# Optimization experiments

Measured on AMD Instinct MI355X. Metric: run time of the kernel, lower is better.

Reference implementation:

```python
import jax, jax.numpy as jnp
import numpy as np

B, N, D_IN, D_OUT = 2, 4096, 768, 768


def setup_inputs() -> dict:
    key = jax.random.key(0)
    kx, kq, kk, kv = jax.random.split(key, 4)
    x = jax.random.normal(kx, (B, N, D_IN), dtype=jnp.float32)
    # Linear(d_in, d_out, bias=False) weights, stored as [d_in, d_out]
    scale = 1.0 / np.sqrt(D_IN)
    Wq = jax.random.normal(kq, (D_IN, D_OUT), dtype=jnp.float32) * scale
    Wk = jax.random.normal(kk, (D_IN, D_OUT), dtype=jnp.float32) * scale
    Wv = jax.random.normal(kv, (D_IN, D_OUT), dtype=jnp.float32) * scale
    return {"x": x, "Wq": Wq, "Wk": Wk, "Wv": Wv}


def reference(x, Wq, Wk, Wv):
    # q,k,v: [B, N, D_OUT]
    q = jnp.einsum('bnd,de->bne', x, Wq)
    k = jnp.einsum('bnd,de->bne', x, Wk)
    v = jnp.einsum('bnd,de->bne', x, Wv)
    # Full [B, N, N] score matrix (naive attention, as in source).
    # NOTE: source's masked_fill is non-in-place and discarded, so NO causal
    # mask is actually applied -- reproduced faithfully here.
    scores = jnp.einsum('bqe,bke->bqk', q, k) / jnp.sqrt(jnp.float32(k.shape[-1]))
    weights = jax.nn.softmax(scores, axis=-1)
    # dropout rate 0.0 / eval mode -> identity
    out = jnp.einsum('bqk,bke->bqe', weights, v)  # [B, N, D_OUT]
    return out
```

## Files before the change

kernel.cpp:

```cpp
#include <hip/hip_runtime.h>

typedef __bf16 bf16x8 __attribute__((ext_vector_type(8)));
typedef float f32x4 __attribute__((ext_vector_type(4)));
typedef unsigned short us8 __attribute__((ext_vector_type(8)));

#define GAS __attribute__((address_space(1)))
#define LAS __attribute__((address_space(3)))

__device__ __forceinline__ unsigned short f32_to_bf16(float f) {
    unsigned int u = __float_as_uint(f);
    u += 0x7FFFu + ((u >> 16) & 1u);
    return (unsigned short)(u >> 16);
}

__device__ __forceinline__ float bf16_to_f32(unsigned short h) {
    return __uint_as_float((unsigned int)h << 16);
}

__device__ __forceinline__ void load16(const unsigned short* g, unsigned short* l) {
    __builtin_amdgcn_global_load_lds((GAS unsigned int*)g, (LAS unsigned int*)l, 16, 0, 0);
}

__global__ __launch_bounds__(1024) void prep(
    const float* __restrict__ x, unsigned short* __restrict__ Xbf,
    const float* __restrict__ W0, const float* __restrict__ W1, const float* __restrict__ W2,
    unsigned short* __restrict__ T0, unsigned short* __restrict__ T1, unsigned short* __restrict__ T2)
{
    __shared__ float tile[32][33];
    const int id = blockIdx.x;
    const int t = threadIdx.x;
    if (id < 1536) {
        int i = id * 1024 + t;
        float4 v = ((const float4*)x)[i];
        ushort4 o;
        o.x = f32_to_bf16(v.x); o.y = f32_to_bf16(v.y);
        o.z = f32_to_bf16(v.z); o.w = f32_to_bf16(v.w);
        ((ushort4*)Xbf)[i] = o;
    } else {
        const int tid = id - 1536;
        const int z = tid / 576, rem = tid % 576;
        const int by = rem / 24, bx = rem % 24;
        const float* W = (z == 0) ? W0 : (z == 1) ? W1 : W2;
        unsigned short* T = (z == 0) ? T0 : (z == 1) ? T1 : T2;
        const int r0 = by * 32, c0 = bx * 32;
        const int tx = t & 31, ty = t >> 5;
        tile[ty][tx] = W[(size_t)(r0 + ty) * 768 + c0 + tx];
        __syncthreads();
        T[(size_t)(c0 + ty) * 768 + r0 + tx] = f32_to_bf16(tile[tx][ty]);
    }
}

template <typename CT>
__global__ __launch_bounds__(256) void gemm_nt(
    const unsigned short* __restrict__ A, const unsigned short* __restrict__ B,
    CT* __restrict__ C, int K, int lda, int ldb, int ldc,
    size_t sA, size_t sB, size_t sC, float alpha)
{
    A += (size_t)blockIdx.z * sA;
    B += (size_t)blockIdx.z * sB;
    C += (size_t)blockIdx.z * sC;
    const int m0 = blockIdx.y * 128;
    const int n0 = blockIdx.x * 128;
    const int t = threadIdx.x;
    const int lane = t & 63;
    const int w = t >> 6;
    const int wm = (w >> 1) * 64;
    const int wn = (w & 1) * 64;

    __shared__ unsigned short At[128 * 64];
    __shared__ unsigned short Bt[128 * 64];

    f32x4 acc[4][4];
#pragma unroll
    for (int i = 0; i < 4; ++i)
#pragma unroll
        for (int j = 0; j < 4; ++j) acc[i][j] = (f32x4){0.f, 0.f, 0.f, 0.f};

    const int r15 = lane & 15;
    const int qa = lane >> 4;

    for (int k0 = 0; k0 < K; k0 += 64) {
#pragma unroll
        for (int i = 0; i < 4; ++i) {
            const int c = i * 256 + t;
            const int row = c >> 3;
            const int cc = (c & 7) ^ (row & 7);
            load16(A + (size_t)(m0 + row) * lda + k0 + cc * 8, &At[c * 8]);
            load16(B + (size_t)(n0 + row) * ldb + k0 + cc * 8, &Bt[c * 8]);
        }
        __syncthreads();

#pragma unroll
        for (int ks = 0; ks < 2; ++ks) {
            bf16x8 af[4], bf[4];
#pragma unroll
            for (int mi = 0; mi < 4; ++mi) {
                const int row = wm + mi * 16 + r15;
                af[mi] = *(const bf16x8*)&At[row * 64 + (((ks << 2) + qa) ^ (row & 7)) * 8];
            }
#pragma unroll
            for (int ni = 0; ni < 4; ++ni) {
                const int row = wn + ni * 16 + r15;
                bf[ni] = *(const bf16x8*)&Bt[row * 64 + (((ks << 2) + qa) ^ (row & 7)) * 8];
            }
#pragma unroll
            for (int mi = 0; mi < 4; ++mi)
#pragma unroll
                for (int ni = 0; ni < 4; ++ni)
                    acc[mi][ni] = __builtin_amdgcn_mfma_f32_16x16x32_bf16(
                        af[mi], bf[ni], acc[mi][ni], 0, 0, 0);
        }
        __syncthreads();
    }

    const int cr = (lane >> 4) * 4;
#pragma unroll
    for (int mi = 0; mi < 4; ++mi) {
#pragma unroll
        for (int ni = 0; ni < 4; ++ni) {
            const int gm = m0 + wm + mi * 16 + cr;
            const int gn = n0 + wn + ni * 16 + r15;
#pragma unroll
            for (int r = 0; r < 4; ++r) {
                float v = alpha * acc[mi][ni][r];
                if constexpr (sizeof(CT) == 2)
                    C[(size_t)(gm + r) * ldc + gn] = (CT)f32_to_bf16(v);
                else
                    C[(size_t)(gm + r) * ldc + gn] = v;
            }
        }
    }
}

template <int NT, int BN64, bool EXP>
__device__ __forceinline__ void gemm256_core(
    const unsigned short* __restrict__ A, const unsigned short* __restrict__ B,
    unsigned short* __restrict__ C,
    int m0, int n0, int lda, int ldb, int ldc, float alpha)
{
    constexpr int BN = BN64 * 64;
    __shared__ unsigned short As[2][256 * 64];
    __shared__ unsigned short Bs[2][BN * 64];

    const int t = threadIdx.x;
    const int lane = t & 63;
    const int w = t >> 6;
    const int wm = (w >> 2) * 128;
    const int wn = (w & 3) * (BN / 4);
    const int r15 = lane & 15;
    const int qa = lane >> 4;

    const unsigned short* srcA[4];
    int dstA[4];
#pragma unroll
    for (int i = 0; i < 4; ++i) {
        const int c = i * 512 + t;
        const int row = c >> 3;
        const int cc = (c & 7) ^ (row & 7);
        srcA[i] = A + (size_t)(m0 + row) * lda + cc * 8;
        dstA[i] = c * 8;
    }
    const unsigned short* srcB[BN64];
    int dstB[BN64];
#pragma unroll
    for (int i = 0; i < BN64; ++i) {
        const int c = i * 512 + t;
        const int row = c >> 3;
        const int cc = (c & 7) ^ (row & 7);
        srcB[i] = B + (size_t)(n0 + row) * ldb + cc * 8;
        dstB[i] = c * 8;
    }

    auto stage = [&](int buf, int kbase) {
#pragma unroll
        for (int i = 0; i < 4; ++i)
            load16(srcA[i] + kbase, &As[buf][dstA[i]]);
#pragma unroll
        for (int i = 0; i < BN64; ++i)
            load16(srcB[i] + kbase, &Bs[buf][dstB[i]]);
    };

    int offA[8][2], offB[BN64][2];
#pragma unroll
    for (int mi = 0; mi < 8; ++mi) {
        const int row = wm + mi * 16 + r15;
#pragma unroll
        for (int ks = 0; ks < 2; ++ks)
            offA[mi][ks] = row * 64 + (((ks << 2) + qa) ^ (row & 7)) * 8;
    }
#pragma unroll
    for (int ni = 0; ni < BN64; ++ni) {
        const int row = wn + ni * 16 + r15;
#pragma unroll
        for (int ks = 0; ks < 2; ++ks)
            offB[ni][ks] = row * 64 + (((ks << 2) + qa) ^ (row & 7)) * 8;
    }

    f32x4 acc[8][BN64];
#pragma unroll
    for (int i = 0; i < 8; ++i)
#pragma unroll
        for (int j = 0; j < BN64; ++j) acc[i][j] = (f32x4){0.f, 0.f, 0.f, 0.f};

    stage(0, 0);
    stage(1, 64);

    for (int tt = 0; tt < NT; ++tt) {
        const int b = tt & 1;

        if (tt == NT - 1) {
            asm volatile("s_waitcnt vmcnt(0)" ::: "memory");
        } else if constexpr (BN64 == 4) {
            asm volatile("s_waitcnt vmcnt(8)" ::: "memory");
        } else {
            asm volatile("s_waitcnt vmcnt(7)" ::: "memory");
        }
        __builtin_amdgcn_s_barrier();

#pragma unroll
        for (int ks = 0; ks < 2; ++ks) {
            bf16x8 aA[8], bB[BN64];
#pragma unroll
            for (int i = 0; i < 8; ++i)
                aA[i] = *(const bf16x8*)&As[b][offA[i][ks]];
#pragma unroll
            for (int ni = 0; ni < BN64; ++ni)
                bB[ni] = *(const bf16x8*)&Bs[b][offB[ni][ks]];
#pragma unroll
            for (int i = 0; i < 8; ++i)
#pragma unroll
                for (int ni = 0; ni < BN64; ++ni)
                    acc[i][ni] = __builtin_amdgcn_mfma_f32_16x16x32_bf16(
                        aA[i], bB[ni], acc[i][ni], 0, 0, 0);
        }

        asm volatile("" ::: "memory");
        __builtin_amdgcn_s_barrier();

        if (tt + 2 < NT) stage(b, (tt + 2) << 6);
    }

    const int cr = (lane >> 4) * 4;
#pragma unroll
    for (int mi = 0; mi < 8; ++mi) {
#pragma unroll
        for (int ni = 0; ni < BN64; ++ni) {
            const int gm = m0 + wm + mi * 16 + cr;
            const int gn = n0 + wn + ni * 16 + r15;
#pragma unroll
            for (int r = 0; r < 4; ++r) {
                float v = alpha * acc[mi][ni][r];
                if constexpr (EXP) v = __expf(v);
                C[(size_t)(gm + r) * ldc + gn] = f32_to_bf16(v);
            }
        }
    }
}

__global__ __launch_bounds__(512, 2) void gemm_s_exp2(
    const unsigned short* __restrict__ Q, const unsigned short* __restrict__ Kb,
    unsigned short* __restrict__ Sexp, float alpha)
{
    const int f = blockIdx.x;
    const int xcd = f & 7;
    const int local = f >> 3;
    const int x = (xcd & 1) * 8 + (local & 7);
    const int y = ((xcd >> 1) & 1) * 8 + (local >> 3);
    const int bb = xcd >> 2;
    const unsigned short* A = Q + (size_t)bb * 3145728;
    const unsigned short* B = Kb + (size_t)bb * 3145728;
    unsigned short* C = Sexp + (size_t)bb * 16777216;
    gemm256_core<12, 4, true>(A, B, C, y * 256, x * 256, 768, 768, 4096, alpha);
}

__global__ __launch_bounds__(512, 2) void gemm_splitk2(
    const unsigned short* __restrict__ P, const unsigned short* __restrict__ Vt,
    unsigned short* __restrict__ Part)
{
    const int f = blockIdx.x;
    const int xcd = f & 7;
    const int local = f >> 3;
    const int j = local & 3;
    const int y = (xcd & 1) * 8 + (local >> 2);
    const int z = xcd >> 1;
    const int batch = z & 1;
    const int split = z >> 1;
    const unsigned short* A = P + (size_t)batch * 16777216 + (size_t)split * 2048;
    const unsigned short* B = Vt + (size_t)batch * 4096 + (size_t)split * 2048;
    unsigned short* C = Part + (size_t)z * 3145728;
    gemm256_core<32, 3, false>(A, B, C, y * 256, j * 192, 4096, 8192, 768, 1.0f);
}

__global__ __launch_bounds__(256) void reduce_norm_rows(
    const unsigned short* __restrict__ Sexp, const unsigned short* __restrict__ Part,
    float* __restrict__ out)
{
    const int g = blockIdx.x;
    const int batch = g >> 12;
    const int r = g & 4095;
    const int t = threadIdx.x;
    const int wv = t >> 6, ln = t & 63;

    const unsigned short* srow = Sexp + (size_t)batch * 16777216 + (size_t)r * 4096;
    us8 a = ((const us8*)srow)[t];
    us8 b = ((const us8*)srow)[t + 256];
    float s = 0.f;
#pragma unroll
    for (int j = 0; j < 8; ++j) s += bf16_to_f32(a[j]) + bf16_to_f32(b[j]);
#pragma unroll
    for (int off = 32; off > 0; off >>= 1) s += __shfl_down(s, off, 64);
    __shared__ float red[4];
    if (ln == 0) red[wv] = s;
    __syncthreads();
    const float inv = 1.f / (red[0] + red[1] + red[2] + red[3]);

    if (t < 192) {
        const int c = t * 4;
        float4 acc = {0.f, 0.f, 0.f, 0.f};
#pragma unroll
        for (int sgroup = 0; sgroup < 2; ++sgroup) {
            const unsigned short* p = Part
                + ((size_t)(sgroup * 2 + batch) * 4096 + r) * 768 + c;
            ushort4 u = *(const ushort4*)p;
            acc.x += bf16_to_f32(u.x);
            acc.y += bf16_to_f32(u.y);
            acc.z += bf16_to_f32(u.z);
            acc.w += bf16_to_f32(u.w);
        }
        float4 o;
        o.x = acc.x * inv; o.y = acc.y * inv; o.z = acc.z * inv; o.w = acc.w * inv;
        *(float4*)(out + (size_t)g * 768 + c) = o;
    }
}

extern "C" void kernel_launch(void* const* d_in, const int* in_sizes, int n_in,
                              void* d_out, int out_size, void* d_ws, size_t ws_size,
                              hipStream_t stream) {
    const float* x  = (const float*)d_in[0];
    const float* Wq = (const float*)d_in[1];
    const float* Wk = (const float*)d_in[2];
    const float* Wv = (const float*)d_in[3];
    float* out = (float*)d_out;

    char* base = (char*)d_ws;
    size_t off = 0;
    auto alloc = [&](size_t b) { char* p = base + off; off += (b + 255) & ~(size_t)255; return p; };

    unsigned short* Xbf = (unsigned short*)alloc(8192ull * 768 * 2);
    unsigned short* WqT = (unsigned short*)alloc(768ull * 768 * 2);
    unsigned short* WkT = (unsigned short*)alloc(768ull * 768 * 2);
    unsigned short* WvT = (unsigned short*)alloc(768ull * 768 * 2);
    unsigned short* Qb  = (unsigned short*)alloc(8192ull * 768 * 2);
    unsigned short* Kb  = (unsigned short*)alloc(8192ull * 768 * 2);
    unsigned short* Vt  = (unsigned short*)alloc(768ull * 8192 * 2);
    unsigned short* Sexp = (unsigned short*)alloc(2ull * 4096 * 4096 * 2);
    unsigned short* Part = (unsigned short*)alloc(4ull * 3145728 * 2);
    (void)ws_size; (void)in_sizes; (void)n_in; (void)out_size; (void)WkT;

    prep<<<dim3(3264), dim3(1024), 0, stream>>>(x, Xbf, Wq, Wk, Wv, WqT, WkT, WvT);
    gemm_nt<unsigned short><<<dim3(6, 64, 2), dim3(256), 0, stream>>>(
        Xbf, WqT, Qb, 768, 768, 768, 768,
         0,  589824,  6291456, 1.0f);
    gemm_nt<unsigned short><<<dim3(64, 6, 1), dim3(256), 0, stream>>>(
        WvT, Xbf, Vt, 768, 768, 768, 8192, 0, 0, 0, 1.0f);
    gemm_s_exp2<<<dim3(512), dim3(512), 0, stream>>>(
        Qb, Kb, Sexp, 0.03608439182435161f);
    gemm_splitk2<<<dim3(256), dim3(512), 0, stream>>>(Sexp, Vt, Part);
    reduce_norm_rows<<<dim3(8192), dim3(256), 0, stream>>>(Sexp, Part, out);
}
```

Baseline: 252.2 us.

## Fuse row-sum into score GEMM, drop split-K and reduce kernel

The softmax row sums are now accumulated with atomics in the exp-score GEMM epilogue, so the separate reduce pass no longer re-reads the full score matrix. The PV GEMM drops split-K and the bf16 partial buffers, running the full K loop with 128x192 tiles and a triple-buffered pipeline, and it applies the normalization directly when writing fp32 output. The Q/K and V projection GEMMs are merged into a single launch, and prep zeroes the lsum buffer. In exchange, the PV GEMM has only 256 blocks with long K loops and fewer waves per block, and the atomics make the row sums order-nondeterministic.

```diff
diff --git a/kernel.cpp b/kernel.cpp
--- a/kernel.cpp
+++ b/kernel.cpp
@@ -24,7 +24,8 @@
 __global__ __launch_bounds__(1024) void prep(
     const float* __restrict__ x, unsigned short* __restrict__ Xbf,
     const float* __restrict__ W0, const float* __restrict__ W1, const float* __restrict__ W2,
-    unsigned short* __restrict__ T0, unsigned short* __restrict__ T1, unsigned short* __restrict__ T2)
+    unsigned short* __restrict__ T0, unsigned short* __restrict__ T1, unsigned short* __restrict__ T2,
+    float* __restrict__ lsum)
 {
     __shared__ float tile[32][33];
     const int id = blockIdx.x;
@@ -36,7 +37,7 @@
         o.x = f32_to_bf16(v.x); o.y = f32_to_bf16(v.y);
         o.z = f32_to_bf16(v.z); o.w = f32_to_bf16(v.w);
         ((ushort4*)Xbf)[i] = o;
-    } else {
+    } else if (id < 3264) {
         const int tid = id - 1536;
         const int z = tid / 576, rem = tid % 576;
         const int by = rem / 24, bx = rem % 24;
@@ -47,20 +48,35 @@
         tile[ty][tx] = W[(size_t)(r0 + ty) * 768 + c0 + tx];
         __syncthreads();
         T[(size_t)(c0 + ty) * 768 + r0 + tx] = f32_to_bf16(tile[tx][ty]);
-    }
-}
-
-template <typename CT>
-__global__ __launch_bounds__(256) void gemm_nt(
-    const unsigned short* __restrict__ A, const unsigned short* __restrict__ B,
-    CT* __restrict__ C, int K, int lda, int ldb, int ldc,
-    size_t sA, size_t sB, size_t sC, float alpha)
+    } else {
+        float4 z4 = {0.f, 0.f, 0.f, 0.f};
+        ((float4*)lsum)[t] = z4;
+        ((float4*)lsum)[t + 1024] = z4;
+    }
+}
+
+__global__ __launch_bounds__(256) void qkv_proj(
+    const unsigned short* __restrict__ Xbf,
+    const unsigned short* __restrict__ Wt,
+    unsigned short* __restrict__ QK,
+    unsigned short* __restrict__ Vt)
 {
-    A += (size_t)blockIdx.z * sA;
-    B += (size_t)blockIdx.z * sB;
-    C += (size_t)blockIdx.z * sC;
-    const int m0 = blockIdx.y * 128;
-    const int n0 = blockIdx.x * 128;
+    const int id = blockIdx.x;
+    const unsigned short* A; const unsigned short* B;
+    unsigned short* C; int ldc, m0, n0;
+    if (id < 768) {
+        const int z = id / 384, r = id % 384;
+        A = Xbf; B = Wt + (size_t)z * 589824; C = QK + (size_t)z * 6291456;
+        ldc = 768;
+        m0 = (r / 6) * 128; n0 = (r % 6) * 128;
+    } else {
+        const int j = id - 768;
+        A = Wt + 1179648ull;
+        B = Xbf; C = Vt;
+        ldc = 8192;
+        m0 = (j >> 6) * 128; n0 = (j & 63) * 128;
+    }
+    const int lda = 768, ldb = 768;
     const int t = threadIdx.x;
     const int lane = t & 63;
     const int w = t >> 6;
@@ -74,12 +90,12 @@
 #pragma unroll
     for (int i = 0; i < 4; ++i)
 #pragma unroll
-        for (int j = 0; j < 4; ++j) acc[i][j] = (f32x4){0.f, 0.f, 0.f, 0.f};
+        for (int j2 = 0; j2 < 4; ++j2) acc[i][j2] = (f32x4){0.f, 0.f, 0.f, 0.f};
 
     const int r15 = lane & 15;
     const int qa = lane >> 4;
 
-    for (int k0 = 0; k0 < K; k0 += 64) {
+    for (int k0 = 0; k0 < 768; k0 += 64) {
 #pragma unroll
         for (int i = 0; i < 4; ++i) {
             const int c = i * 256 + t;
@@ -115,151 +131,20 @@
 
     const int cr = (lane >> 4) * 4;
 #pragma unroll
-    for (int mi = 0; mi < 4; ++mi) {
+    for (int mi = 0; mi < 4; ++mi)
 #pragma unroll
         for (int ni = 0; ni < 4; ++ni) {
             const int gm = m0 + wm + mi * 16 + cr;
             const int gn = n0 + wn + ni * 16 + r15;
 #pragma unroll
-            for (int r = 0; r < 4; ++r) {
-                float v = alpha * acc[mi][ni][r];
-                if constexpr (sizeof(CT) == 2)
-                    C[(size_t)(gm + r) * ldc + gn] = (CT)f32_to_bf16(v);
-                else
-                    C[(size_t)(gm + r) * ldc + gn] = v;
-            }
-        }
-    }
-}
-
-template <int NT, int BN64, bool EXP>
-__device__ __forceinline__ void gemm256_core(
-    const unsigned short* __restrict__ A, const unsigned short* __restrict__ B,
-    unsigned short* __restrict__ C,
-    int m0, int n0, int lda, int ldb, int ldc, float alpha)
-{
-    constexpr int BN = BN64 * 64;
-    __shared__ unsigned short As[2][256 * 64];
-    __shared__ unsigned short Bs[2][BN * 64];
-
-    const int t = threadIdx.x;
-    const int lane = t & 63;
-    const int w = t >> 6;
-    const int wm = (w >> 2) * 128;
-    const int wn = (w & 3) * (BN / 4);
-    const int r15 = lane & 15;
-    const int qa = lane >> 4;
-
-    const unsigned short* srcA[4];
-    int dstA[4];
-#pragma unroll
-    for (int i = 0; i < 4; ++i) {
-        const int c = i * 512 + t;
-        const int row = c >> 3;
-        const int cc = (c & 7) ^ (row & 7);
-        srcA[i] = A + (size_t)(m0 + row) * lda + cc * 8;
-        dstA[i] = c * 8;
-    }
-    const unsigned short* srcB[BN64];
-    int dstB[BN64];
-#pragma unroll
-    for (int i = 0; i < BN64; ++i) {
-        const int c = i * 512 + t;
-        const int row = c >> 3;
-        const int cc = (c & 7) ^ (row & 7);
-        srcB[i] = B + (size_t)(n0 + row) * ldb + cc * 8;
-        dstB[i] = c * 8;
-    }
-
-    auto stage = [&](int buf, int kbase) {
-#pragma unroll
-        for (int i = 0; i < 4; ++i)
-            load16(srcA[i] + kbase, &As[buf][dstA[i]]);
-#pragma unroll
-        for (int i = 0; i < BN64; ++i)
-            load16(srcB[i] + kbase, &Bs[buf][dstB[i]]);
-    };
-
-    int offA[8][2], offB[BN64][2];
-#pragma unroll
-    for (int mi = 0; mi < 8; ++mi) {
-        const int row = wm + mi * 16 + r15;
-#pragma unroll
-        for (int ks = 0; ks < 2; ++ks)
-            offA[mi][ks] = row * 64 + (((ks << 2) + qa) ^ (row & 7)) * 8;
-    }
-#pragma unroll
-    for (int ni = 0; ni < BN64; ++ni) {
-        const int row = wn + ni * 16 + r15;
-#pragma unroll
-        for (int ks = 0; ks < 2; ++ks)
-            offB[ni][ks] = row * 64 + (((ks << 2) + qa) ^ (row & 7)) * 8;
-    }
-
-    f32x4 acc[8][BN64];
-#pragma unroll
-    for (int i = 0; i < 8; ++i)
-#pragma unroll
-        for (int j = 0; j < BN64; ++j) acc[i][j] = (f32x4){0.f, 0.f, 0.f, 0.f};
-
-    stage(0, 0);
-    stage(1, 64);
-
-    for (int tt = 0; tt < NT; ++tt) {
-        const int b = tt & 1;
-
-        if (tt == NT - 1) {
-            asm volatile("s_waitcnt vmcnt(0)" ::: "memory");
-        } else if constexpr (BN64 == 4) {
-            asm volatile("s_waitcnt vmcnt(8)" ::: "memory");
-        } else {
-            asm volatile("s_waitcnt vmcnt(7)" ::: "memory");
-        }
-        __builtin_amdgcn_s_barrier();
-
-#pragma unroll
-        for (int ks = 0; ks < 2; ++ks) {
-            bf16x8 aA[8], bB[BN64];
-#pragma unroll
-            for (int i = 0; i < 8; ++i)
-                aA[i] = *(const bf16x8*)&As[b][offA[i][ks]];
-#pragma unroll
-            for (int ni = 0; ni < BN64; ++ni)
-                bB[ni] = *(const bf16x8*)&Bs[b][offB[ni][ks]];
-#pragma unroll
-            for (int i = 0; i < 8; ++i)
-#pragma unroll
-                for (int ni = 0; ni < BN64; ++ni)
-                    acc[i][ni] = __builtin_amdgcn_mfma_f32_16x16x32_bf16(
-                        aA[i], bB[ni], acc[i][ni], 0, 0, 0);
-        }
-
-        asm volatile("" ::: "memory");
-        __builtin_amdgcn_s_barrier();
-
-        if (tt + 2 < NT) stage(b, (tt + 2) << 6);
-    }
-
-    const int cr = (lane >> 4) * 4;
-#pragma unroll
-    for (int mi = 0; mi < 8; ++mi) {
-#pragma unroll
-        for (int ni = 0; ni < BN64; ++ni) {
-            const int gm = m0 + wm + mi * 16 + cr;
-            const int gn = n0 + wn + ni * 16 + r15;
-#pragma unroll
-            for (int r = 0; r < 4; ++r) {
-                float v = alpha * acc[mi][ni][r];
-                if constexpr (EXP) v = __expf(v);
-                C[(size_t)(gm + r) * ldc + gn] = f32_to_bf16(v);
-            }
-        }
-    }
+            for (int r = 0; r < 4; ++r)
+                C[(size_t)(gm + r) * ldc + gn] = f32_to_bf16(acc[mi][ni][r]);
+        }
 }
 
 __global__ __launch_bounds__(512, 2) void gemm_s_exp2(
     const unsigned short* __restrict__ Q, const unsigned short* __restrict__ Kb,
-    unsigned short* __restrict__ Sexp, float alpha)
+    unsigned short* __restrict__ Sexp, float* __restrict__ lsum, float alpha)
 {
     const int f = blockIdx.x;
     const int xcd = f & 7;
@@ -270,66 +155,270 @@
     const unsigned short* A = Q + (size_t)bb * 3145728;
     const unsigned short* B = Kb + (size_t)bb * 3145728;
     unsigned short* C = Sexp + (size_t)bb * 16777216;
-    gemm256_core<12, 4, true>(A, B, C, y * 256, x * 256, 768, 768, 4096, alpha);
-}
-
-__global__ __launch_bounds__(512, 2) void gemm_splitk2(
+    float* ls = lsum + bb * 4096;
+    const int m0 = y * 256, n0 = x * 256;
+    const int lda = 768, ldb = 768, ldc = 4096;
+    constexpr int NT = 12;
+
+    __shared__ unsigned short As[2][256 * 64];
+    __shared__ unsigned short Bs[2][256 * 64];
+
+    const int t = threadIdx.x;
+    const int lane = t & 63;
+    const int w = t >> 6;
+    const int wm = (w >> 2) * 128;
+    const int wn = (w & 3) * 64;
+    const int r15 = lane & 15;
+    const int qa = lane >> 4;
+
+    const unsigned short* srcA[4];
+    const unsigned short* srcB[4];
+    int dst[4];
+#pragma unroll
+    for (int i = 0; i < 4; ++i) {
+        const int c = i * 512 + t;
+        const int row = c >> 3;
+        const int cc = (c & 7) ^ (row & 7);
+        srcA[i] = A + (size_t)(m0 + row) * lda + cc * 8;
+        srcB[i] = B + (size_t)(n0 + row) * ldb + cc * 8;
+        dst[i] = c * 8;
+    }
+
+    auto stage = [&](int buf, int kbase) {
+#pragma unroll
+        for (int i = 0; i < 4; ++i)
+            load16(srcA[i] + kbase, &As[buf][dst[i]]);
+#pragma unroll
+        for (int i = 0; i < 4; ++i)
+            load16(srcB[i] + kbase, &Bs[buf][dst[i]]);
+    };
+
+    int offA[8][2], offB[4][2];
+#pragma unroll
+    for (int mi = 0; mi < 8; ++mi) {
+        const int row = wm + mi * 16 + r15;
+#pragma unroll
+        for (int ks = 0; ks < 2; ++ks)
+            offA[mi][ks] = row * 64 + (((ks << 2) + qa) ^ (row & 7)) * 8;
+    }
+#pragma unroll
+    for (int ni = 0; ni < 4; ++ni) {
+        const int row = wn + ni * 16 + r15;
+#pragma unroll
+        for (int ks = 0; ks < 2; ++ks)
+            offB[ni][ks] = row * 64 + (((ks << 2) + qa) ^ (row & 7)) * 8;
+    }
+
+    f32x4 acc[8][4];
+#pragma unroll
+    for (int i = 0; i < 8; ++i)
+#pragma unroll
+        for (int j = 0; j < 4; ++j) acc[i][j] = (f32x4){0.f, 0.f, 0.f, 0.f};
+
+    stage(0, 0);
+    stage(1, 64);
+
+    for (int tt = 0; tt < NT; ++tt) {
+        const int b = tt & 1;
+        if (tt == NT - 1) {
+            asm volatile("s_waitcnt vmcnt(0)" ::: "memory");
+        } else {
+            asm volatile("s_waitcnt vmcnt(8)" ::: "memory");
+        }
+        __builtin_amdgcn_s_barrier();
+
+#pragma unroll
+        for (int ks = 0; ks < 2; ++ks) {
+            bf16x8 aA[8], bB[4];
+#pragma unroll
+            for (int i = 0; i < 8; ++i)
+                aA[i] = *(const bf16x8*)&As[b][offA[i][ks]];
+#pragma unroll
+            for (int ni = 0; ni < 4; ++ni)
+                bB[ni] = *(const bf16x8*)&Bs[b][offB[ni][ks]];
+#pragma unroll
+            for (int i = 0; i < 8; ++i)
+#pragma unroll
+                for (int ni = 0; ni < 4; ++ni)
+                    acc[i][ni] = __builtin_amdgcn_mfma_f32_16x16x32_bf16(
+                        aA[i], bB[ni], acc[i][ni], 0, 0, 0);
+        }
+
+        asm volatile("" ::: "memory");
+        __builtin_amdgcn_s_barrier();
+
+        if (tt + 2 < NT) stage(b, (tt + 2) << 6);
+    }
+
+    const int cr = (lane >> 4) * 4;
+#pragma unroll
+    for (int mi = 0; mi < 8; ++mi) {
+        const int gm = m0 + wm + mi * 16 + cr;
+        float rs0 = 0.f, rs1 = 0.f, rs2 = 0.f, rs3 = 0.f;
+#pragma unroll
+        for (int ni = 0; ni < 4; ++ni) {
+            const int gn = n0 + wn + ni * 16 + r15;
+            float v0 = __expf(alpha * acc[mi][ni][0]);
+            float v1 = __expf(alpha * acc[mi][ni][1]);
+            float v2 = __expf(alpha * acc[mi][ni][2]);
+            float v3 = __expf(alpha * acc[mi][ni][3]);
+            C[(size_t)(gm + 0) * ldc + gn] = f32_to_bf16(v0);
+            C[(size_t)(gm + 1) * ldc + gn] = f32_to_bf16(v1);
+            C[(size_t)(gm + 2) * ldc + gn] = f32_to_bf16(v2);
+            C[(size_t)(gm + 3) * ldc + gn] = f32_to_bf16(v3);
+            rs0 += v0; rs1 += v1; rs2 += v2; rs3 += v3;
+        }
+#pragma unroll
+        for (int m = 1; m < 16; m <<= 1) {
+            rs0 += __shfl_xor(rs0, m, 64);
+            rs1 += __shfl_xor(rs1, m, 64);
+            rs2 += __shfl_xor(rs2, m, 64);
+            rs3 += __shfl_xor(rs3, m, 64);
+        }
+        if (r15 == 0) {
+            atomicAdd(&ls[gm + 0], rs0);
+            atomicAdd(&ls[gm + 1], rs1);
+            atomicAdd(&ls[gm + 2], rs2);
+            atomicAdd(&ls[gm + 3], rs3);
+        }
+    }
+}
+
+__global__ __launch_bounds__(512, 2) void gemm_out(
     const unsigned short* __restrict__ P, const unsigned short* __restrict__ Vt,
-    unsigned short* __restrict__ Part)
+    const float* __restrict__ lsum, float* __restrict__ out)
 {
     const int f = blockIdx.x;
     const int xcd = f & 7;
-    const int local = f >> 3;
-    const int j = local & 3;
-    const int y = (xcd & 1) * 8 + (local >> 2);
-    const int z = xcd >> 1;
-    const int batch = z & 1;
-    const int split = z >> 1;
-    const unsigned short* A = P + (size_t)batch * 16777216 + (size_t)split * 2048;
-    const unsigned short* B = Vt + (size_t)batch * 4096 + (size_t)split * 2048;
-    unsigned short* C = Part + (size_t)z * 3145728;
-    gemm256_core<32, 3, false>(A, B, C, y * 256, j * 192, 4096, 8192, 768, 1.0f);
-}
-
-__global__ __launch_bounds__(256) void reduce_norm_rows(
-    const unsigned short* __restrict__ Sexp, const unsigned short* __restrict__ Part,
-    float* __restrict__ out)
-{
-    const int g = blockIdx.x;
-    const int batch = g >> 12;
-    const int r = g & 4095;
+    const int batch = xcd >> 2;
+    const int nb = xcd & 3;
+    const int mb = f >> 3;
+    const unsigned short* A = P + (size_t)batch * 16777216;
+    const unsigned short* B = Vt + (size_t)batch * 4096;
+    const float* ls = lsum + batch * 4096;
+    float* C = out + (size_t)batch * 3145728;
+    const int m0 = mb * 128, n0 = nb * 192;
+    const int lda = 4096, ldb = 8192;
+    constexpr int NT = 64;
+
+    __shared__ unsigned short As[3][128 * 64];
+    __shared__ unsigned short Bs[3][192 * 64];
+
     const int t = threadIdx.x;
-    const int wv = t >> 6, ln = t & 63;
-
-    const unsigned short* srow = Sexp + (size_t)batch * 16777216 + (size_t)r * 4096;
-    us8 a = ((const us8*)srow)[t];
-    us8 b = ((const us8*)srow)[t + 256];
-    float s = 0.f;
-#pragma unroll
-    for (int j = 0; j < 8; ++j) s += bf16_to_f32(a[j]) + bf16_to_f32(b[j]);
-#pragma unroll
-    for (int off = 32; off > 0; off >>= 1) s += __shfl_down(s, off, 64);
-    __shared__ float red[4];
-    if (ln == 0) red[wv] = s;
-    __syncthreads();
-    const float inv = 1.f / (red[0] + red[1] + red[2] + red[3]);
-
-    if (t < 192) {
-        const int c = t * 4;
-        float4 acc = {0.f, 0.f, 0.f, 0.f};
-#pragma unroll
-        for (int sgroup = 0; sgroup < 2; ++sgroup) {
-            const unsigned short* p = Part
-                + ((size_t)(sgroup * 2 + batch) * 4096 + r) * 768 + c;
-            ushort4 u = *(const ushort4*)p;
-            acc.x += bf16_to_f32(u.x);
-            acc.y += bf16_to_f32(u.y);
-            acc.z += bf16_to_f32(u.z);
-            acc.w += bf16_to_f32(u.w);
-        }
-        float4 o;
-        o.x = acc.x * inv; o.y = acc.y * inv; o.z = acc.z * inv; o.w = acc.w * inv;
-        *(float4*)(out + (size_t)g * 768 + c) = o;
+    const int lane = t & 63;
+    const int w = t >> 6;
+    const int wm = (w >> 2) * 64;
+    const int wn = (w & 3) * 48;
+    const int r15 = lane & 15;
+    const int qa = lane >> 4;
+
+    const unsigned short* srcA[2];
+    int dstA[2];
+#pragma unroll
+    for (int i = 0; i < 2; ++i) {
+        const int c = i * 512 + t;
+        const int row = c >> 3;
+        const int cc = (c & 7) ^ (row & 7);
+        srcA[i] = A + (size_t)(m0 + row) * lda + cc * 8;
+        dstA[i] = c * 8;
+    }
+    const unsigned short* srcB[3];
+    int dstB[3];
+#pragma unroll
+    for (int i = 0; i < 3; ++i) {
+        const int c = i * 512 + t;
+        const int row = c >> 3;
+        const int cc = (c & 7) ^ (row & 7);
+        srcB[i] = B + (size_t)(n0 + row) * ldb + cc * 8;
+        dstB[i] = c * 8;
+    }
+
+    auto stage = [&](int buf, int kbase) {
+#pragma unroll
+        for (int i = 0; i < 2; ++i)
+            load16(srcA[i] + kbase, &As[buf][dstA[i]]);
+#pragma unroll
+        for (int i = 0; i < 3; ++i)
+            load16(srcB[i] + kbase, &Bs[buf][dstB[i]]);
+    };
+
+    int offA[4][2], offB[3][2];
+#pragma unroll
+    for (int mi = 0; mi < 4; ++mi) {
+        const int row = wm + mi * 16 + r15;
+#pragma unroll
+        for (int ks = 0; ks < 2; ++ks)
+            offA[mi][ks] = row * 64 + (((ks << 2) + qa) ^ (row & 7)) * 8;
+    }
+#pragma unroll
+    for (int ni = 0; ni < 3; ++ni) {
+        const int row = wn + ni * 16 + r15;
+#pragma unroll
+        for (int ks = 0; ks < 2; ++ks)
+            offB[ni][ks] = row * 64 + (((ks << 2) + qa) ^ (row & 7)) * 8;
+    }
+
+    f32x4 acc[4][3];
+#pragma unroll
+    for (int i = 0; i < 4; ++i)
+#pragma unroll
+        for (int j = 0; j < 3; ++j) acc[i][j] = (f32x4){0.f, 0.f, 0.f, 0.f};
+
+    stage(0, 0);
+    stage(1, 64);
+    stage(2, 128);
+
+    int b = 0;
+    for (int tt = 0; tt < NT; ++tt) {
+        if (tt < NT - 2) {
+            asm volatile("s_waitcnt vmcnt(10)" ::: "memory");
+        } else if (tt == NT - 2) {
+            asm volatile("s_waitcnt vmcnt(5)" ::: "memory");
+        } else {
+            asm volatile("s_waitcnt vmcnt(0)" ::: "memory");
+        }
+        __builtin_amdgcn_s_barrier();
+
+#pragma unroll
+        for (int ks = 0; ks < 2; ++ks) {
+            bf16x8 aA[4], bB[3];
+#pragma unroll
+            for (int i = 0; i < 4; ++i)
+                aA[i] = *(const bf16x8*)&As[b][offA[i][ks]];
+#pragma unroll
+            for (int ni = 0; ni < 3; ++ni)
+                bB[ni] = *(const bf16x8*)&Bs[b][offB[ni][ks]];
+#pragma unroll
+            for (int i = 0; i < 4; ++i)
+#pragma unroll
+                for (int ni = 0; ni < 3; ++ni)
+                    acc[i][ni] = __builtin_amdgcn_mfma_f32_16x16x32_bf16(
+                        aA[i], bB[ni], acc[i][ni], 0, 0, 0);
+        }
+
+        asm volatile("" ::: "memory");
+        __builtin_amdgcn_s_barrier();
+
+        if (tt + 3 < NT) stage(b, (tt + 3) << 6);
+        b = (b == 2) ? 0 : b + 1;
+    }
+
+    const int cr = (lane >> 4) * 4;
+#pragma unroll
+    for (int mi = 0; mi < 4; ++mi) {
+        const int gm = m0 + wm + mi * 16 + cr;
+        const float i0 = 1.f / ls[gm + 0];
+        const float i1 = 1.f / ls[gm + 1];
+        const float i2 = 1.f / ls[gm + 2];
+        const float i3 = 1.f / ls[gm + 3];
+#pragma unroll
+        for (int ni = 0; ni < 3; ++ni) {
+            const int gn = n0 + wn + ni * 16 + r15;
+            C[(size_t)(gm + 0) * 768 + gn] = acc[mi][ni][0] * i0;
+            C[(size_t)(gm + 1) * 768 + gn] = acc[mi][ni][1] * i1;
+            C[(size_t)(gm + 2) * 768 + gn] = acc[mi][ni][2] * i2;
+            C[(size_t)(gm + 3) * 768 + gn] = acc[mi][ni][3] * i3;
+        }
     }
 }
 
@@ -354,17 +443,12 @@
     unsigned short* Kb  = (unsigned short*)alloc(8192ull * 768 * 2);
     unsigned short* Vt  = (unsigned short*)alloc(768ull * 8192 * 2);
     unsigned short* Sexp = (unsigned short*)alloc(2ull * 4096 * 4096 * 2);
-    unsigned short* Part = (unsigned short*)alloc(4ull * 3145728 * 2);
-    (void)ws_size; (void)in_sizes; (void)n_in; (void)out_size; (void)WkT;
-
-    prep<<<dim3(3264), dim3(1024), 0, stream>>>(x, Xbf, Wq, Wk, Wv, WqT, WkT, WvT);
-    gemm_nt<unsigned short><<<dim3(6, 64, 2), dim3(256), 0, stream>>>(
-        Xbf, WqT, Qb, 768, 768, 768, 768,
-         0,  589824,  6291456, 1.0f);
-    gemm_nt<unsigned short><<<dim3(64, 6, 1), dim3(256), 0, stream>>>(
-        WvT, Xbf, Vt, 768, 768, 768, 8192, 0, 0, 0, 1.0f);
+    float* lsum = (float*)alloc(2ull * 4096 * 4);
+    (void)ws_size; (void)in_sizes; (void)n_in; (void)out_size; (void)WkT; (void)WvT;
+
+    prep<<<dim3(3265), dim3(1024), 0, stream>>>(x, Xbf, Wq, Wk, Wv, WqT, WkT, WvT, lsum);
+    qkv_proj<<<dim3(1152), dim3(256), 0, stream>>>(Xbf, WqT, Qb, Vt);
     gemm_s_exp2<<<dim3(512), dim3(512), 0, stream>>>(
-        Qb, Kb, Sexp, 0.03608439182435161f);
-    gemm_splitk2<<<dim3(256), dim3(512), 0, stream>>>(Sexp, Vt, Part);
-    reduce_norm_rows<<<dim3(8192), dim3(256), 0, stream>>>(Sexp, Part, out);
-}
+        Qb, Kb, Sexp, lsum, 0.03608439182435161f);
+    gemm_out<<<dim3(256), dim3(512), 0, stream>>>(Sexp, Vt, lsum, out);
+}
```

New measurement: 271.9 us. 1.08x slower.
